# Kernel tuning notes

Hardware: AMD Instinct MI355X
Metric: run time of the kernel (lower is better)

## Reference

```python
import jax, jax.numpy as jnp
import numpy as np

N_P, N_A, D, H, E = 200000, 100000, 64, 32, 1000000


def setup_inputs() -> dict:
    key = jax.random.key(0)
    ks = jax.random.split(key, 32)
    inp = {}
    inp["x_paper"] = jax.random.normal(ks[0], (N_P, D), jnp.float32)
    inp["x_author"] = jax.random.normal(ks[1], (N_A, D), jnp.float32)
    inp["cites_src"] = jax.random.randint(ks[2], (E,), 0, N_P, jnp.int32)
    inp["cites_dst"] = jax.random.randint(ks[3], (E,), 0, N_P, jnp.int32)
    inp["writes_src"] = jax.random.randint(ks[4], (E,), 0, N_A, jnp.int32)
    inp["writes_dst"] = jax.random.randint(ks[5], (E,), 0, N_P, jnp.int32)
    inp["rev_src"] = jax.random.randint(ks[6], (E,), 0, N_P, jnp.int32)
    inp["rev_dst"] = jax.random.randint(ks[7], (E,), 0, N_A, jnp.int32)
    # per-relation SAGEConv params; layer 1: D->H, layer 2: H->H
    i = 8
    for layer, din in ((1, D), (2, H)):
        for rel in ("cites", "writes", "rev"):
            inp[f"W{layer}l_{rel}"] = 0.1 * jax.random.normal(ks[i], (din, H), jnp.float32); i += 1
            inp[f"W{layer}r_{rel}"] = 0.1 * jax.random.normal(ks[i], (din, H), jnp.float32); i += 1
            inp[f"b{layer}_{rel}"] = 0.01 * jax.random.normal(ks[i], (H,), jnp.float32); i += 1
    return inp


def _sage(x_src, x_dst, src, dst, Wl, Wr, b, n_dst):
    # PyG SAGEConv (aggr='mean'): lin_l(mean of source msgs) + lin_r(x_dst) + bias
    msg = x_src[src]                                              # [E, d] gather
    s = jax.ops.segment_sum(msg, dst, num_segments=n_dst)         # [n_dst, d]
    cnt = jax.ops.segment_sum(jnp.ones((src.shape[0],), x_src.dtype), dst, num_segments=n_dst)
    mean = s / jnp.maximum(cnt, 1.0)[:, None]
    return mean @ Wl + x_dst @ Wr + b


def reference(x_paper, x_author, cites_src, cites_dst, writes_src, writes_dst,
              rev_src, rev_dst,
              W1l_cites, W1r_cites, b1_cites, W1l_writes, W1r_writes, b1_writes,
              W1l_rev, W1r_rev, b1_rev,
              W2l_cites, W2r_cites, b2_cites, W2l_writes, W2r_writes, b2_writes,
              W2l_rev, W2r_rev, b2_rev):
    n_p, n_a = x_paper.shape[0], x_author.shape[0]
    # layer 1 (to_hetero sums relation outputs per dst node type), then relu
    p1 = jax.nn.relu(
        _sage(x_paper, x_paper, cites_src, cites_dst, W1l_cites, W1r_cites, b1_cites, n_p)
        + _sage(x_author, x_paper, writes_src, writes_dst, W1l_writes, W1r_writes, b1_writes, n_p))
    a1 = jax.nn.relu(
        _sage(x_paper, x_author, rev_src, rev_dst, W1l_rev, W1r_rev, b1_rev, n_a))
    # layer 2, return 'paper' output (no activation)
    p2 = (_sage(p1, p1, cites_src, cites_dst, W2l_cites, W2r_cites, b2_cites, n_p)
          + _sage(a1, p1, writes_src, writes_dst, W2l_writes, W2r_writes, b2_writes, n_p))
    return p2
```

## Files before the change

kernel.cpp:

```cpp
#include <hip/hip_runtime.h>

typedef unsigned short u16;
typedef unsigned int   u32;
typedef unsigned char  u8;
typedef __attribute__((ext_vector_type(8))) short bf16x8;
typedef __attribute__((ext_vector_type(4))) float f32x4;

#define N_P 200000
#define N_A 100000
#define DD  64
#define HH  32
#define NE  1000000
#define NBP 782
#define NBA 391
#define NB4K 245
#define NCB 196
#define P4CAP 8192
#define NB_P16 12500
#define NB_A16 6250
#define NB4K3 735

__device__ inline float bf2f(u16 u) { return __uint_as_float(((u32)u) << 16); }
__device__ inline u16 f2bf(float f) {
    u32 u = __float_as_uint(f);
    u += 0x7fffu + ((u >> 16) & 1u);
    return (u16)(u >> 16);
}
__device__ inline float lo_f(u32 m) { return __uint_as_float(m << 16); }
__device__ inline float hi_f(u32 m) { return __uint_as_float(m & 0xffff0000u); }
__device__ inline u32 cvtpk(float a, float b) {
    u32 r;
    asm("v_cvt_pk_bf16_f32 %0, %1, %2" : "=v"(r) : "v"(a), "v"(b));
    return r;
}

__device__ inline void gseg_dual(
    const u16* __restrict__ yA, const int* __restrict__ bkA, int s0, int e0,
    const u16* __restrict__ yB, const int* __restrict__ bkB, int s1, int e1,
    int lane, float& axo, float& ayo, float& bxo, float& byo) {
    float ax = 0.f, ay = 0.f, bx = 0.f, by = 0.f;
    int lastA = min(max(e0 - 1, s0), NE - 1);
    int lastB = min(max(e1 - 1, s1), NE - 1);
    for (int j0 = s0, j1 = s1; (j0 < e0) || (j1 < e1); j0 += 8, j1 += 8) {
        int ia[8], ib[8];
#pragma unroll
        for (int i = 0; i < 8; ++i) ia[i] = bkA[min(j0 + i, lastA)];
#pragma unroll
        for (int i = 0; i < 8; ++i) ib[i] = bkB[min(j1 + i, lastB)];
        u32 ma[8], mb[8];
#pragma unroll
        for (int i = 0; i < 8; ++i)
            ma[i] = *(const u32*)(yA + (size_t)(u32)ia[i] + lane * 2);
#pragma unroll
        for (int i = 0; i < 8; ++i)
            mb[i] = *(const u32*)(yB + (size_t)(u32)ib[i] + lane * 2);
#pragma unroll
        for (int i = 0; i < 8; ++i) {
            u32 va = (j0 + i < e0) ? ma[i] : 0u;
            ax += lo_f(va); ay += hi_f(va);
        }
#pragma unroll
        for (int i = 0; i < 8; ++i) {
            u32 vb = (j1 + i < e1) ? mb[i] : 0u;
            bx += lo_f(vb); by += hi_f(vb);
        }
    }
    axo = ax; ayo = ay; bxo = bx; byo = by;
}

__global__ __launch_bounds__(256) void p1_hist_k(
    const int* __restrict__ cd, const int* __restrict__ wd, const int* __restrict__ rd,
    int* __restrict__ gsizes) {
    int rel = blockIdx.y;
    const int* dst; int shift;
    if (rel == 0)      { dst = cd; shift = 10; }
    else if (rel == 1) { dst = wd; shift = 10; }
    else               { dst = rd; shift = 9;  }
    __shared__ int cnt[256];
    int t = threadIdx.x;
    cnt[t] = 0;
    __syncthreads();
    int e0 = blockIdx.x * 4096;
    if (e0 + 4096 <= NE) {
        const int4* dv = (const int4*)(dst + e0);
#pragma unroll
        for (int i = 0; i < 4; ++i) {
            int4 v = dv[i * 256 + t];
            atomicAdd(&cnt[v.x >> shift], 1);
            atomicAdd(&cnt[v.y >> shift], 1);
            atomicAdd(&cnt[v.z >> shift], 1);
            atomicAdd(&cnt[v.w >> shift], 1);
        }
    } else {
#pragma unroll
        for (int i = 0; i < 16; ++i) {
            int e = e0 + i * 256 + t;
            if (e < NE) atomicAdd(&cnt[dst[e] >> shift], 1);
        }
    }
    __syncthreads();
    if (t < NCB && cnt[t]) atomicAdd(&gsizes[rel * NCB + t], cnt[t]);
}

__global__ __launch_bounds__(256) void p2_scan_k(
    const int* __restrict__ gsizes, int* __restrict__ bases, int* __restrict__ gcur) {
    __shared__ int lds[256];
    int t = threadIdx.x;
    for (int rel = 0; rel < 3; ++rel) {
        int v = (t < NCB) ? gsizes[rel * NCB + t] : 0;
        lds[t] = v; __syncthreads();
#pragma unroll
        for (int o = 1; o < 256; o <<= 1) {
            int x = (t >= o) ? lds[t - o] : 0;
            __syncthreads();
            lds[t] += x;
            __syncthreads();
        }
        int ex = lds[t] - v;
        if (t < NCB) { bases[rel * NCB + t] = ex; gcur[rel * NCB + t] = ex; }
        __syncthreads();
    }
}

__global__ __launch_bounds__(256) void p3t1_k(
    const int* __restrict__ cs, const int* __restrict__ cd,
    const int* __restrict__ ws_, const int* __restrict__ wd,
    const int* __restrict__ rs, const int* __restrict__ rd,
    int* __restrict__ gcur,
    u32* __restrict__ pr_c, u32* __restrict__ pr_w, u32* __restrict__ pr_r,
    const float* __restrict__ xp, const float* __restrict__ xa,
    const u16* __restrict__ wt1h, const u16* __restrict__ wt1l,
    const float* __restrict__ b1s, const float* __restrict__ b1r,
    u16* __restrict__ y_pc, u16* __restrict__ y_pr, u16* __restrict__ y_aw,
    u16* __restrict__ hb_p, u16* __restrict__ hb_a) {
    __shared__ float smem[256 * 34];
    int t = threadIdx.x;
    if (blockIdx.x < NB4K3) {
        u32* sbuf  = (u32*)smem;
        int* cnt   = (int*)(smem + 4096);
        int* sc    = (int*)(smem + 4352);
        int* lcur  = (int*)(smem + 4608);
        int* gbase = (int*)(smem + 4864);
        u8*  bb    = (u8*)(smem + 5120);
        int rel = blockIdx.x / NB4K;
        int blk = blockIdx.x - rel * NB4K;
        const int *src, *dst; int shift; u32* out;
        if (rel == 0)      { src = cs;  dst = cd; shift = 10; out = pr_c; }
        else if (rel == 1) { src = ws_; dst = wd; shift = 10; out = pr_w; }
        else               { src = rs;  dst = rd; shift = 9;  out = pr_r; }
        cnt[t] = 0;
        __syncthreads();
        int e0 = blk * 4096;
        int myd[16], mys[16];
        if (e0 + 4096 <= NE) {
            const int4* dv = (const int4*)(dst + e0);
            const int4* sv = (const int4*)(src + e0);
#pragma unroll
            for (int i = 0; i < 4; ++i) {
                int4 v = dv[i * 256 + t];
                int4 s = sv[i * 256 + t];
                myd[4 * i] = v.x; myd[4 * i + 1] = v.y; myd[4 * i + 2] = v.z; myd[4 * i + 3] = v.w;
                mys[4 * i] = s.x; mys[4 * i + 1] = s.y; mys[4 * i + 2] = s.z; mys[4 * i + 3] = s.w;
                atomicAdd(&cnt[v.x >> shift], 1);
                atomicAdd(&cnt[v.y >> shift], 1);
                atomicAdd(&cnt[v.z >> shift], 1);
                atomicAdd(&cnt[v.w >> shift], 1);
            }
        } else {
#pragma unroll
            for (int i = 0; i < 4; ++i) {
#pragma unroll
                for (int c = 0; c < 4; ++c) {
                    int e = e0 + (i * 256 + t) * 4 + c;
                    int idx = 4 * i + c;
                    if (e < NE) {
                        myd[idx] = dst[e]; mys[idx] = src[e];
                        atomicAdd(&cnt[myd[idx] >> shift], 1);
                    } else { myd[idx] = -1; mys[idx] = 0; }
                }
            }
        }
        __syncthreads();
        int v = cnt[t];
        sc[t] = v; __syncthreads();
#pragma unroll
        for (int o = 1; o < 256; o <<= 1) {
            int x = (t >= o) ? sc[t - o] : 0;
            __syncthreads();
            sc[t] += x;
            __syncthreads();
        }
        int ex = sc[t] - v;
        __syncthreads();
        sc[t] = ex;
        lcur[t] = ex;
        if (t < NCB) gbase[t] = atomicAdd(&gcur[rel * NCB + t], cnt[t]);
        __syncthreads();
#pragma unroll
        for (int i = 0; i < 16; ++i) {
            if (myd[i] >= 0) {
                int d = myd[i];
                int cb = d >> shift;
                u32 dloc = (u32)(d - (cb << shift));
                u32 pk = (dloc << 18) | (u32)mys[i];
                int p = atomicAdd(&lcur[cb], 1);
                sbuf[p] = pk;
                bb[p] = (u8)cb;
            }
        }
        __syncthreads();
        int nvalid = min(4096, NE - e0);
        for (int i = t; i < nvalid; i += 256) {
            int cb = bb[i];
            out[gbase[cb] + (i - sc[cb])] = sbuf[i];
        }
    } else {
        float* Cs = smem;
        int w = t >> 6, l = t & 63;
        int lm = l & 15, lk = l >> 4;
        int bx = blockIdx.x - NB4K3;
        bool paper = bx < NBP;
        int row0 = (paper ? bx : bx - NBP) * 256;
        const float* x = paper ? xp : xa;
        int NROW = paper ? N_P : N_A;
        int nv = min(256, NROW - row0);
        bf16x8 xh[4][2], xl[4][2];
#pragma unroll
        for (int i = 0; i < 4; ++i) {
            int rowg = min(row0 + w * 64 + i * 16 + lm, NROW - 1);
            const float* rp = x + (size_t)rowg * DD + lk * 8;
#pragma unroll
            for (int kc = 0; kc < 2; ++kc) {
                float4 a = *(const float4*)(rp + kc * 32);
                float4 b = *(const float4*)(rp + kc * 32 + 4);
                float f[8] = {a.x, a.y, a.z, a.w, b.x, b.y, b.z, b.w};
                union { u32 u[4]; bf16x8 v; } H, L;
#pragma unroll
                for (int j = 0; j < 4; ++j) {
                    u32 u0 = __float_as_uint(f[2 * j]);
                    u32 u1 = __float_as_uint(f[2 * j + 1]);
                    u32 m0 = u0 & 0xffff0000u;
                    u32 m1 = u1 & 0xffff0000u;
                    H.u[j] = (u0 >> 16) | m1;
                    float l0 = f[2 * j]     - __uint_as_float(m0);
                    float l1 = f[2 * j + 1] - __uint_as_float(m1);
                    L.u[j] = cvtpk(l0, l1);
                }
                xh[i][kc] = H.v; xl[i][kc] = L.v;
            }
        }
        int nw = paper ? 3 : 2;
#pragma unroll 1
        for (int iw = 0; iw < nw; ++iw) {
            int mat = paper ? iw : (3 + iw);
            const u16* Wh = wt1h + mat * 2048;
            const u16* Wl = wt1l + mat * 2048;
            bf16x8 Bh[2][2], Bl[2][2];
#pragma unroll
            for (int ct = 0; ct < 2; ++ct)
#pragma unroll
                for (int kc = 0; kc < 2; ++kc) {
                    int off = (ct * 16 + lm) * 64 + kc * 32 + lk * 8;
                    Bh[ct][kc] = *(const bf16x8*)(Wh + off);
                    Bl[ct][kc] = *(const bf16x8*)(Wl + off);
                }
            float bv[2] = {0.f, 0.f};
            if (paper && iw == 2)  { bv[0] = b1s[lm]; bv[1] = b1s[16 + lm]; }
            if (!paper && iw == 1) { bv[0] = b1r[lm]; bv[1] = b1r[16 + lm]; }
#pragma unroll
            for (int i = 0; i < 4; ++i) {
#pragma unroll
                for (int ct = 0; ct < 2; ++ct) {
                    f32x4 acc = {bv[ct], bv[ct], bv[ct], bv[ct]};
                    acc = __builtin_amdgcn_mfma_f32_16x16x32_bf16(xh[i][0], Bh[ct][0], acc, 0, 0, 0);
                    acc = __builtin_amdgcn_mfma_f32_16x16x32_bf16(xh[i][1], Bh[ct][1], acc, 0, 0, 0);
                    acc = __builtin_amdgcn_mfma_f32_16x16x32_bf16(xl[i][0], Bh[ct][0], acc, 0, 0, 0);
                    acc = __builtin_amdgcn_mfma_f32_16x16x32_bf16(xl[i][1], Bh[ct][1], acc, 0, 0, 0);
                    acc = __builtin_amdgcn_mfma_f32_16x16x32_bf16(xh[i][0], Bl[ct][0], acc, 0, 0, 0);
                    acc = __builtin_amdgcn_mfma_f32_16x16x32_bf16(xh[i][1], Bl[ct][1], acc, 0, 0, 0);
                    int rbase = w * 64 + i * 16 + lk * 4;
#pragma unroll
                    for (int r = 0; r < 4; ++r)
                        Cs[(rbase + r) * 34 + ct * 16 + lm] = acc[r];
                }
            }
            asm volatile("s_waitcnt lgkmcnt(0)" ::: "memory");
            u16* outp;
            if (paper) outp = (iw == 0) ? y_pc : (iw == 1) ? y_pr : hb_p;
            else       outp = (iw == 0) ? y_aw : hb_a;
            u32* g = (u32*)(outp + (size_t)row0 * HH);
#pragma unroll
            for (int p = 0; p < 4; ++p) {
                int j = p * 64 + l;
                int rl = w * 64 + (j >> 2);
                if (rl < nv) {
                    const float* q = Cs + rl * 34 + (j & 3) * 8;
                    u32 o[4];
#pragma unroll
                    for (int jj = 0; jj < 4; ++jj)
                        o[jj] = cvtpk(q[2 * jj], q[2 * jj + 1]);
                    *(uint4*)(g + ((size_t)w * 256 + j) * 4) = make_uint4(o[0], o[1], o[2], o[3]);
                }
            }
            asm volatile("" ::: "memory");
        }
    }
}

__global__ __launch_bounds__(256) void p4_sort_k(
    const int* __restrict__ bases, const int* __restrict__ gsizes,
    const u32* __restrict__ pr_c, const u32* __restrict__ pr_w, const u32* __restrict__ pr_r,
    int* __restrict__ bkt_c, int* __restrict__ bkt_w, int* __restrict__ bkt_r,
    int* __restrict__ st_c, int* __restrict__ st_w, int* __restrict__ st_r) {
    int rel = blockIdx.y;
    const u32* pr; int* bkt; int* st; int width, n;
    if (rel == 0)      { pr = pr_c; bkt = bkt_c; st = st_c; width = 1024; n = N_P; }
    else if (rel == 1) { pr = pr_w; bkt = bkt_w; st = st_w; width = 1024; n = N_P; }
    else               { pr = pr_r; bkt = bkt_r; st = st_r; width = 512;  n = N_A; }
    __shared__ u32 sin[P4CAP];
    __shared__ int cnt[1024], sc2[1024], tmp[256];
    int t = threadIdx.x;
    int b = blockIdx.x;
    int base = bases[rel * NCB + b];
    int size = min(gsizes[rel * NCB + b], P4CAP);
    int d0 = b * width;
    int nd = min(width, n - d0);
    if (nd <= 0) return;
#pragma unroll
    for (int j = t; j < 1024; j += 256) cnt[j] = 0;
    __syncthreads();
    for (int i = t; i < size; i += 256) {
        u32 pk = pr[base + i];
        sin[i] = pk;
        atomicAdd(&cnt[pk >> 18], 1);
    }
    __syncthreads();
    int j0 = 4 * t;
    int c0 = cnt[j0], c1 = cnt[j0 + 1], c2 = cnt[j0 + 2], c3 = cnt[j0 + 3];
    int tot = c0 + c1 + c2 + c3;
    tmp[t] = tot; __syncthreads();
#pragma unroll
    for (int o = 1; o < 256; o <<= 1) {
        int x = (t >= o) ? tmp[t - o] : 0;
        __syncthreads();
        tmp[t] += x;
        __syncthreads();
    }
    int pre = tmp[t] - tot;
    sc2[j0] = pre;
    sc2[j0 + 1] = pre + c0;
    sc2[j0 + 2] = pre + c0 + c1;
    sc2[j0 + 3] = pre + c0 + c1 + c2;
    __syncthreads();
    for (int j = t; j < nd; j += 256) st[d0 + j] = base + sc2[j];
#pragma unroll
    for (int j = t; j < 1024; j += 256) cnt[j] = 0;
    __syncthreads();
    for (int i = t; i < size; i += 256) {
        u32 pk = sin[i];
        int dl = (int)(pk >> 18);
        int pos = sc2[dl] + atomicAdd(&cnt[dl], 1);
        bkt[base + pos] = (int)((pk & 0x3FFFFu) * HH);
    }
}

__global__ __launch_bounds__(256) void prep_w_k(
    const float* __restrict__ W1lc, const float* __restrict__ W1lr,
    const float* __restrict__ W1rc, const float* __restrict__ W1rw,
    const float* __restrict__ W1lw, const float* __restrict__ W1rr,
    const float* __restrict__ W2lc, const float* __restrict__ W2rc,
    const float* __restrict__ W2rw, const float* __restrict__ W2lw,
    const float* __restrict__ b1c, const float* __restrict__ b1w,
    const float* __restrict__ b2c, const float* __restrict__ b2w,
    u16* __restrict__ wt1h, u16* __restrict__ wt1l,
    u16* __restrict__ wt2h, u16* __restrict__ wt2l,
    float* __restrict__ b1s, float* __restrict__ b2s,
    int* __restrict__ gsizes) {
    int m = blockIdx.x, t = threadIdx.x;
    if (m == 0) {
        for (int e = t; e < 3 * NCB; e += 256) gsizes[e] = 0;
    }
    if (m < 5) {
        const float *A = nullptr, *B = nullptr;
        if (m == 0) A = W1lc;
        else if (m == 1) A = W1lr;
        else if (m == 2) { A = W1rc; B = W1rw; }
        else if (m == 3) A = W1lw;
        else A = W1rr;
        for (int e = t; e < 2048; e += 256) {
            int k = e >> 5, n = e & 31;
            float v = A[e] + (B ? B[e] : 0.f);
            u16 h = f2bf(v);
            u16 lw = f2bf(v - bf2f(h));
            wt1h[m * 2048 + n * 64 + k] = h;
            wt1l[m * 2048 + n * 64 + k] = lw;
        }
        if (m == 2 && t < HH) b1s[t] = b1c[t] + b1w[t];
    } else {
        int mm = m - 5;
        const float *A = nullptr, *B = nullptr;
        if (mm == 0) A = W2lc;
        else if (mm == 1) { A = W2rc; B = W2rw; }
        else A = W2lw;
        for (int e = t; e < 1024; e += 256) {
            int k = e >> 5, n = e & 31;
            float v = A[e] + (B ? B[e] : 0.f);
            u16 h = f2bf(v);
            u16 lw = f2bf(v - bf2f(h));
            wt2h[mm * 1024 + n * 32 + k] = h;
            wt2l[mm * 1024 + n * 32 + k] = lw;
        }
        if (mm == 1 && t < HH) b2s[t] = b2c[t] + b2w[t];
    }
}

__global__ __launch_bounds__(256) void agg1_k(
    const u16* __restrict__ y_pc, const u16* __restrict__ y_aw,
    const u16* __restrict__ y_pr,
    const int* __restrict__ st_c, const int* __restrict__ bkt_c,
    const int* __restrict__ st_w, const int* __restrict__ bkt_w,
    const int* __restrict__ st_r, const int* __restrict__ bkt_r,
    u32* __restrict__ hb_p, u32* __restrict__ hb_a) {
    int t = threadIdx.x, g = t >> 4, lane = t & 15;
    if (blockIdx.x < NB_P16) {
        int row = blockIdx.x * 16 + g;
        u32 self = hb_p[(size_t)row * (HH / 2) + lane];
        int s0 = st_c[row];
        int e0 = (row == N_P - 1) ? NE : st_c[row + 1];
        int s1 = st_w[row];
        int e1 = (row == N_P - 1) ? NE : st_w[row + 1];
        float cx, cy, wx, wy;
        gseg_dual(y_pc, bkt_c, s0, e0, y_aw, bkt_w, s1, e1, lane, cx, cy, wx, wy);
        int d0 = e0 - s0, d1 = e1 - s1;
        float iv0 = 1.0f / (float)(d0 < 1 ? 1 : d0);
        float iv1 = 1.0f / (float)(d1 < 1 ? 1 : d1);
        float ax = fmaxf(cx * iv0 + wx * iv1 + lo_f(self), 0.f);
        float ay = fmaxf(cy * iv0 + wy * iv1 + hi_f(self), 0.f);
        hb_p[(size_t)row * (HH / 2) + lane] = cvtpk(ax, ay);
    } else {
        int row = (blockIdx.x - NB_P16) * 16 + g;
        u32 self = hb_a[(size_t)row * (HH / 2) + lane];
        int s = st_r[row];
        int e = (row == N_A - 1) ? NE : st_r[row + 1];
        int mid = (s + e) >> 1;
        float ax0, ay0, ax1, ay1;
        gseg_dual(y_pr, bkt_r, s, mid, y_pr, bkt_r, mid, e, lane, ax0, ay0, ax1, ay1);
        int dg = e - s;
        float iv = 1.0f / (float)(dg < 1 ? 1 : dg);
        float ax = fmaxf((ax0 + ax1) * iv + lo_f(self), 0.f);
        float ay = fmaxf((ay0 + ay1) * iv + hi_f(self), 0.f);
        hb_a[(size_t)row * (HH / 2) + lane] = cvtpk(ax, ay);
    }
}

__global__ __launch_bounds__(256) void agg2_k(
    const u16* __restrict__ hb_p, const u16* __restrict__ hb_a,
    const int* __restrict__ st_c, const int* __restrict__ bkt_c,
    const int* __restrict__ st_w, const int* __restrict__ bkt_w,
    const u16* __restrict__ wt2h, const u16* __restrict__ wt2l,
    const float* __restrict__ b2s, float* __restrict__ out) {
    __shared__ float mcs[16][34];
    __shared__ float mws[16][34];
    __shared__ float cso[16][34];
    int t = threadIdx.x, g = t >> 4, lane = t & 15;
    int row0 = blockIdx.x * 16;
    int row = row0 + g;
    int s0 = st_c[row];
    int e0 = (row == N_P - 1) ? NE : st_c[row + 1];
    int s1 = st_w[row];
    int e1 = (row == N_P - 1) ? NE : st_w[row + 1];
    float cx, cy, wx, wy;
    gseg_dual(hb_p, bkt_c, s0, e0, hb_a, bkt_w, s1, e1, lane, cx, cy, wx, wy);
    int d0 = e0 - s0, d1 = e1 - s1;
    float iv0 = 1.0f / (float)(d0 < 1 ? 1 : d0);
    float iv1 = 1.0f / (float)(d1 < 1 ? 1 : d1);
    mcs[g][2 * lane] = cx * iv0;  mcs[g][2 * lane + 1] = cy * iv0;
    mws[g][2 * lane] = wx * iv1;  mws[g][2 * lane + 1] = wy * iv1;
    __syncthreads();
    if (t < 64) {
        int lm = t & 15, lk = t >> 4;
        bf16x8 as_ = *(const bf16x8*)(hb_p + (size_t)(row0 + lm) * HH + lk * 8);
        bf16x8 mch, mcl, mwh, mwl;
        {
            union { u32 u[4]; bf16x8 v; } H, L;
#pragma unroll
            for (int j = 0; j < 4; ++j) {
                float f0 = mcs[lm][lk * 8 + 2 * j];
                float f1 = mcs[lm][lk * 8 + 2 * j + 1];
                u32 u0 = __float_as_uint(f0), u1 = __float_as_uint(f1);
                u32 m0 = u0 & 0xffff0000u, m1 = u1 & 0xffff0000u;
                H.u[j] = (u0 >> 16) | m1;
                L.u[j] = cvtpk(f0 - __uint_as_float(m0), f1 - __uint_as_float(m1));
            }
            mch = H.v; mcl = L.v;
#pragma unroll
            for (int j = 0; j < 4; ++j) {
                float f0 = mws[lm][lk * 8 + 2 * j];
                float f1 = mws[lm][lk * 8 + 2 * j + 1];
                u32 u0 = __float_as_uint(f0), u1 = __float_as_uint(f1);
                u32 m0 = u0 & 0xffff0000u, m1 = u1 & 0xffff0000u;
                H.u[j] = (u0 >> 16) | m1;
                L.u[j] = cvtpk(f0 - __uint_as_float(m0), f1 - __uint_as_float(m1));
            }
            mwh = H.v; mwl = L.v;
        }
#pragma unroll
        for (int ct = 0; ct < 2; ++ct) {
            int boff = (ct * 16 + lm) * 32 + lk * 8;
            bf16x8 Bch = *(const bf16x8*)(wt2h + boff);
            bf16x8 Bcl = *(const bf16x8*)(wt2l + boff);
            bf16x8 Bsh = *(const bf16x8*)(wt2h + 1024 + boff);
            bf16x8 Bsl = *(const bf16x8*)(wt2l + 1024 + boff);
            bf16x8 Bwh = *(const bf16x8*)(wt2h + 2048 + boff);
            bf16x8 Bwl = *(const bf16x8*)(wt2l + 2048 + boff);
            float bb = b2s[ct * 16 + lm];
            f32x4 acc = {bb, bb, bb, bb};
            acc = __builtin_amdgcn_mfma_f32_16x16x32_bf16(as_, Bsh, acc, 0, 0, 0);
            acc = __builtin_amdgcn_mfma_f32_16x16x32_bf16(as_, Bsl, acc, 0, 0, 0);
            acc = __builtin_amdgcn_mfma_f32_16x16x32_bf16(mch, Bch, acc, 0, 0, 0);
            acc = __builtin_amdgcn_mfma_f32_16x16x32_bf16(mcl, Bch, acc, 0, 0, 0);
            acc = __builtin_amdgcn_mfma_f32_16x16x32_bf16(mch, Bcl, acc, 0, 0, 0);
            acc = __builtin_amdgcn_mfma_f32_16x16x32_bf16(mwh, Bwh, acc, 0, 0, 0);
            acc = __builtin_amdgcn_mfma_f32_16x16x32_bf16(mwl, Bwh, acc, 0, 0, 0);
            acc = __builtin_amdgcn_mfma_f32_16x16x32_bf16(mwh, Bwl, acc, 0, 0, 0);
#pragma unroll
            for (int r = 0; r < 4; ++r)
                cso[lk * 4 + r][ct * 16 + lm] = acc[r];
        }
    }
    __syncthreads();
    int r = t >> 4, c = (t & 15) * 2;
    *(float2*)(out + (size_t)(row0 + r) * HH + c) = make_float2(cso[r][c], cso[r][c + 1]);
}

extern "C" void kernel_launch(void* const* d_in, const int* in_sizes, int n_in,
                              void* d_out, int out_size, void* d_ws, size_t ws_size,
                              hipStream_t stream) {
    const float* x_p  = (const float*)d_in[0];
    const float* x_a  = (const float*)d_in[1];
    const int* c_src  = (const int*)d_in[2];
    const int* c_dst  = (const int*)d_in[3];
    const int* w_src  = (const int*)d_in[4];
    const int* w_dst  = (const int*)d_in[5];
    const int* r_src  = (const int*)d_in[6];
    const int* r_dst  = (const int*)d_in[7];
    const float* W1l_c = (const float*)d_in[8];
    const float* W1r_c = (const float*)d_in[9];
    const float* b1_c  = (const float*)d_in[10];
    const float* W1l_w = (const float*)d_in[11];
    const float* W1r_w = (const float*)d_in[12];
    const float* b1_w  = (const float*)d_in[13];
    const float* W1l_r = (const float*)d_in[14];
    const float* W1r_r = (const float*)d_in[15];
    const float* b1_r  = (const float*)d_in[16];
    const float* W2l_c = (const float*)d_in[17];
    const float* W2r_c = (const float*)d_in[18];
    const float* b2_c  = (const float*)d_in[19];
    const float* W2l_w = (const float*)d_in[20];
    const float* W2r_w = (const float*)d_in[21];
    const float* b2_w  = (const float*)d_in[22];

    int* gsizes = (int*)d_ws;
    int* bases  = gsizes + 3 * NCB;
    int* gcur   = bases + 3 * NCB;
    int* st_c   = gcur + 3 * NCB;
    int* st_w   = st_c + N_P;
    int* st_r   = st_w + N_P;
    int* bkt_c  = st_r + N_A;
    int* bkt_w  = bkt_c + NE;
    int* bkt_r  = bkt_w + NE;
    u16* wt1h  = (u16*)(bkt_r + NE);
    u16* wt1l  = wt1h + 5 * 2048;
    u16* wt2h  = wt1l + 5 * 2048;
    u16* wt2l  = wt2h + 3 * 1024;
    float* b1s = (float*)(wt2l + 3 * 1024);
    float* b2s = b1s + HH;
    u16* hb_p  = (u16*)(b2s + HH);
    u16* hb_a  = hb_p + (size_t)N_P * HH;
    u16* y_pc  = hb_a + (size_t)N_A * HH;
    u16* y_pr  = y_pc + (size_t)N_P * HH;
    u16* y_aw  = y_pr + (size_t)N_P * HH;
    float* tail = (float*)(y_aw + (size_t)N_A * HH);
    u32* pr_c  = (u32*)tail;
    u32* pr_w  = pr_c + NE;
    u32* pr_r  = pr_w + NE;
    float* outp = (float*)d_out;

    const size_t need = ((uintptr_t)(pr_r + NE)) - (uintptr_t)d_ws;
    if (ws_size < need) return;

    prep_w_k<<<8, 256, 0, stream>>>(W1l_c, W1l_r, W1r_c, W1r_w, W1l_w, W1r_r,
                                    W2l_c, W2r_c, W2r_w, W2l_w,
                                    b1_c, b1_w, b2_c, b2_w,
                                    wt1h, wt1l, wt2h, wt2l, b1s, b2s, gsizes);
    p1_hist_k<<<dim3(NB4K, 3), 256, 0, stream>>>(c_dst, w_dst, r_dst, gsizes);
    p2_scan_k<<<1, 256, 0, stream>>>(gsizes, bases, gcur);
    p3t1_k<<<NB4K3 + NBP + NBA, 256, 0, stream>>>(
        c_src, c_dst, w_src, w_dst, r_src, r_dst, gcur, pr_c, pr_w, pr_r,
        x_p, x_a, wt1h, wt1l, b1s, b1_r, y_pc, y_pr, y_aw, hb_p, hb_a);
    p4_sort_k<<<dim3(NCB, 3), 256, 0, stream>>>(bases, gsizes, pr_c, pr_w, pr_r,
                                                bkt_c, bkt_w, bkt_r, st_c, st_w, st_r);
    agg1_k<<<NB_P16 + NB_A16, 256, 0, stream>>>(y_pc, y_aw, y_pr,
                                                st_c, bkt_c, st_w, bkt_w, st_r, bkt_r,
                                                (u32*)hb_p, (u32*)hb_a);
    agg2_k<<<NB_P16, 256, 0, stream>>>(hb_p, hb_a, st_c, bkt_c, st_w, bkt_w,
                                       wt2h, wt2l, b2s, outp);
}
```

Baseline: 363.6 us.

## Widen sort blocks, parallelize scan per relation, add CSR sentinel, fast-path full gathers

The per-bucket counting sort now runs with 1024 threads per block instead of 256, which raises parallelism in the LDS histogram and scatter phases. The prefix-scan kernel runs one block per relation instead of looping serially, and it writes an end sentinel into each CSR start array. With the sentinel, the aggregation kernels drop the last-row branch. The gather loop gains an unclamped, unmasked fast path for full 8-edge chunks, cutting min/select work in the common case at the cost of more code size.

Result: no change. 367.9 us (+1.2%).

```diff
diff --git a/kernel.cpp b/kernel.cpp
--- a/kernel.cpp
+++ b/kernel.cpp
@@ -42,11 +42,22 @@
     int lastA = min(max(e0 - 1, s0), NE - 1);
     int lastB = min(max(e1 - 1, s1), NE - 1);
     for (int j0 = s0, j1 = s1; (j0 < e0) || (j1 < e1); j0 += 8, j1 += 8) {
+        bool fA = (j0 + 8 <= e0), fB = (j1 + 8 <= e1);
         int ia[8], ib[8];
-#pragma unroll
-        for (int i = 0; i < 8; ++i) ia[i] = bkA[min(j0 + i, lastA)];
-#pragma unroll
-        for (int i = 0; i < 8; ++i) ib[i] = bkB[min(j1 + i, lastB)];
+        if (fA) {
+#pragma unroll
+            for (int i = 0; i < 8; ++i) ia[i] = bkA[j0 + i];
+        } else {
+#pragma unroll
+            for (int i = 0; i < 8; ++i) ia[i] = bkA[min(j0 + i, lastA)];
+        }
+        if (fB) {
+#pragma unroll
+            for (int i = 0; i < 8; ++i) ib[i] = bkB[j1 + i];
+        } else {
+#pragma unroll
+            for (int i = 0; i < 8; ++i) ib[i] = bkB[min(j1 + i, lastB)];
+        }
         u32 ma[8], mb[8];
 #pragma unroll
         for (int i = 0; i < 8; ++i)
@@ -54,15 +65,25 @@
 #pragma unroll
         for (int i = 0; i < 8; ++i)
             mb[i] = *(const u32*)(yB + (size_t)(u32)ib[i] + lane * 2);
-#pragma unroll
-        for (int i = 0; i < 8; ++i) {
-            u32 va = (j0 + i < e0) ? ma[i] : 0u;
-            ax += lo_f(va); ay += hi_f(va);
-        }
-#pragma unroll
-        for (int i = 0; i < 8; ++i) {
-            u32 vb = (j1 + i < e1) ? mb[i] : 0u;
-            bx += lo_f(vb); by += hi_f(vb);
+        if (fA) {
+#pragma unroll
+            for (int i = 0; i < 8; ++i) { ax += lo_f(ma[i]); ay += hi_f(ma[i]); }
+        } else {
+#pragma unroll
+            for (int i = 0; i < 8; ++i) {
+                u32 va = (j0 + i < e0) ? ma[i] : 0u;
+                ax += lo_f(va); ay += hi_f(va);
+            }
+        }
+        if (fB) {
+#pragma unroll
+            for (int i = 0; i < 8; ++i) { bx += lo_f(mb[i]); by += hi_f(mb[i]); }
+        } else {
+#pragma unroll
+            for (int i = 0; i < 8; ++i) {
+                u32 vb = (j1 + i < e1) ? mb[i] : 0u;
+                bx += lo_f(vb); by += hi_f(vb);
+            }
         }
     }
     axo = ax; ayo = ay; bxo = bx; byo = by;
@@ -103,22 +124,26 @@
 }
 
 __global__ __launch_bounds__(256) void p2_scan_k(
-    const int* __restrict__ gsizes, int* __restrict__ bases, int* __restrict__ gcur) {
+    const int* __restrict__ gsizes, int* __restrict__ bases, int* __restrict__ gcur,
+    int* __restrict__ st_c, int* __restrict__ st_w, int* __restrict__ st_r) {
     __shared__ int lds[256];
     int t = threadIdx.x;
-    for (int rel = 0; rel < 3; ++rel) {
-        int v = (t < NCB) ? gsizes[rel * NCB + t] : 0;
-        lds[t] = v; __syncthreads();
-#pragma unroll
-        for (int o = 1; o < 256; o <<= 1) {
-            int x = (t >= o) ? lds[t - o] : 0;
-            __syncthreads();
-            lds[t] += x;
-            __syncthreads();
-        }
-        int ex = lds[t] - v;
-        if (t < NCB) { bases[rel * NCB + t] = ex; gcur[rel * NCB + t] = ex; }
-        __syncthreads();
+    int rel = blockIdx.x;
+    int v = (t < NCB) ? gsizes[rel * NCB + t] : 0;
+    lds[t] = v; __syncthreads();
+#pragma unroll
+    for (int o = 1; o < 256; o <<= 1) {
+        int x = (t >= o) ? lds[t - o] : 0;
+        __syncthreads();
+        lds[t] += x;
+        __syncthreads();
+    }
+    int ex = lds[t] - v;
+    if (t < NCB) { bases[rel * NCB + t] = ex; gcur[rel * NCB + t] = ex; }
+    if (t == 0) {
+        if (rel == 0)      st_c[N_P] = NE;
+        else if (rel == 1) st_w[N_P] = NE;
+        else               st_r[N_A] = NE;
     }
 }
 
@@ -307,7 +332,7 @@
     }
 }
 
-__global__ __launch_bounds__(256) void p4_sort_k(
+__global__ __launch_bounds__(1024) void p4_sort_k(
     const int* __restrict__ bases, const int* __restrict__ gsizes,
     const u32* __restrict__ pr_c, const u32* __restrict__ pr_w, const u32* __restrict__ pr_r,
     int* __restrict__ bkt_c, int* __restrict__ bkt_w, int* __restrict__ bkt_r,
@@ -326,37 +351,41 @@
     int d0 = b * width;
     int nd = min(width, n - d0);
     if (nd <= 0) return;
-#pragma unroll
-    for (int j = t; j < 1024; j += 256) cnt[j] = 0;
-    __syncthreads();
-    for (int i = t; i < size; i += 256) {
+    cnt[t] = 0;
+    __syncthreads();
+    for (int i = t; i < size; i += 1024) {
         u32 pk = pr[base + i];
         sin[i] = pk;
         atomicAdd(&cnt[pk >> 18], 1);
     }
     __syncthreads();
-    int j0 = 4 * t;
-    int c0 = cnt[j0], c1 = cnt[j0 + 1], c2 = cnt[j0 + 2], c3 = cnt[j0 + 3];
-    int tot = c0 + c1 + c2 + c3;
-    tmp[t] = tot; __syncthreads();
+    int c0 = 0, c1 = 0, c2 = 0, c3 = 0, tot = 0, j0 = 0;
+    if (t < 256) {
+        j0 = 4 * t;
+        c0 = cnt[j0]; c1 = cnt[j0 + 1]; c2 = cnt[j0 + 2]; c3 = cnt[j0 + 3];
+        tot = c0 + c1 + c2 + c3;
+        tmp[t] = tot;
+    }
+    __syncthreads();
 #pragma unroll
     for (int o = 1; o < 256; o <<= 1) {
-        int x = (t >= o) ? tmp[t - o] : 0;
-        __syncthreads();
-        tmp[t] += x;
-        __syncthreads();
-    }
-    int pre = tmp[t] - tot;
-    sc2[j0] = pre;
-    sc2[j0 + 1] = pre + c0;
-    sc2[j0 + 2] = pre + c0 + c1;
-    sc2[j0 + 3] = pre + c0 + c1 + c2;
-    __syncthreads();
-    for (int j = t; j < nd; j += 256) st[d0 + j] = base + sc2[j];
-#pragma unroll
-    for (int j = t; j < 1024; j += 256) cnt[j] = 0;
-    __syncthreads();
-    for (int i = t; i < size; i += 256) {
+        int x = (t >= o && t < 256) ? tmp[t - o] : 0;
+        __syncthreads();
+        if (t < 256) tmp[t] += x;
+        __syncthreads();
+    }
+    if (t < 256) {
+        int pre = tmp[t] - tot;
+        sc2[j0] = pre;
+        sc2[j0 + 1] = pre + c0;
+        sc2[j0 + 2] = pre + c0 + c1;
+        sc2[j0 + 3] = pre + c0 + c1 + c2;
+    }
+    __syncthreads();
+    for (int j = t; j < nd; j += 1024) st[d0 + j] = base + sc2[j];
+    cnt[t] = 0;
+    __syncthreads();
+    for (int i = t; i < size; i += 1024) {
         u32 pk = sin[i];
         int dl = (int)(pk >> 18);
         int pos = sc2[dl] + atomicAdd(&cnt[dl], 1);
@@ -425,10 +454,8 @@
     if (blockIdx.x < NB_P16) {
         int row = blockIdx.x * 16 + g;
         u32 self = hb_p[(size_t)row * (HH / 2) + lane];
-        int s0 = st_c[row];
-        int e0 = (row == N_P - 1) ? NE : st_c[row + 1];
-        int s1 = st_w[row];
-        int e1 = (row == N_P - 1) ? NE : st_w[row + 1];
+        int s0 = st_c[row], e0 = st_c[row + 1];
+        int s1 = st_w[row], e1 = st_w[row + 1];
         float cx, cy, wx, wy;
         gseg_dual(y_pc, bkt_c, s0, e0, y_aw, bkt_w, s1, e1, lane, cx, cy, wx, wy);
         int d0 = e0 - s0, d1 = e1 - s1;
@@ -440,8 +467,7 @@
     } else {
         int row = (blockIdx.x - NB_P16) * 16 + g;
         u32 self = hb_a[(size_t)row * (HH / 2) + lane];
-        int s = st_r[row];
-        int e = (row == N_A - 1) ? NE : st_r[row + 1];
+        int s = st_r[row], e = st_r[row + 1];
         int mid = (s + e) >> 1;
         float ax0, ay0, ax1, ay1;
         gseg_dual(y_pr, bkt_r, s, mid, y_pr, bkt_r, mid, e, lane, ax0, ay0, ax1, ay1);
@@ -465,10 +491,8 @@
     int t = threadIdx.x, g = t >> 4, lane = t & 15;
     int row0 = blockIdx.x * 16;
     int row = row0 + g;
-    int s0 = st_c[row];
-    int e0 = (row == N_P - 1) ? NE : st_c[row + 1];
-    int s1 = st_w[row];
-    int e1 = (row == N_P - 1) ? NE : st_w[row + 1];
+    int s0 = st_c[row], e0 = st_c[row + 1];
+    int s1 = st_w[row], e1 = st_w[row + 1];
     float cx, cy, wx, wy;
     gseg_dual(hb_p, bkt_c, s0, e0, hb_a, bkt_w, s1, e1, lane, cx, cy, wx, wy);
     int d0 = e0 - s0, d1 = e1 - s1;
@@ -564,9 +588,9 @@
     int* bases  = gsizes + 3 * NCB;
     int* gcur   = bases + 3 * NCB;
     int* st_c   = gcur + 3 * NCB;
-    int* st_w   = st_c + N_P;
-    int* st_r   = st_w + N_P;
-    int* bkt_c  = st_r + N_A;
+    int* st_w   = st_c + N_P + 1;
+    int* st_r   = st_w + N_P + 1;
+    int* bkt_c  = st_r + N_A + 1;
     int* bkt_w  = bkt_c + NE;
     int* bkt_r  = bkt_w + NE;
     u16* wt1h  = (u16*)(bkt_r + NE);
@@ -594,12 +618,12 @@
                                     b1_c, b1_w, b2_c, b2_w,
                                     wt1h, wt1l, wt2h, wt2l, b1s, b2s, gsizes);
     p1_hist_k<<<dim3(NB4K, 3), 256, 0, stream>>>(c_dst, w_dst, r_dst, gsizes);
-    p2_scan_k<<<1, 256, 0, stream>>>(gsizes, bases, gcur);
+    p2_scan_k<<<3, 256, 0, stream>>>(gsizes, bases, gcur, st_c, st_w, st_r);
     p3t1_k<<<NB4K3 + NBP + NBA, 256, 0, stream>>>(
         c_src, c_dst, w_src, w_dst, r_src, r_dst, gcur, pr_c, pr_w, pr_r,
         x_p, x_a, wt1h, wt1l, b1s, b1_r, y_pc, y_pr, y_aw, hb_p, hb_a);
-    p4_sort_k<<<dim3(NCB, 3), 256, 0, stream>>>(bases, gsizes, pr_c, pr_w, pr_r,
-                                                bkt_c, bkt_w, bkt_r, st_c, st_w, st_r);
+    p4_sort_k<<<dim3(NCB, 3), 1024, 0, stream>>>(bases, gsizes, pr_c, pr_w, pr_r,
+                                                 bkt_c, bkt_w, bkt_r, st_c, st_w, st_r);
     agg1_k<<<NB_P16 + NB_A16, 256, 0, stream>>>(y_pc, y_aw, y_pr,
                                                 st_c, bkt_c, st_w, bkt_w, st_r, bkt_r,
                                                 (u32*)hb_p, (u32*)hb_a);
```
